# Optimization experiments

Measured on AMD Instinct MI355X. Metric: run time of the kernel, lower is better.

Reference implementation:

```python
import jax, jax.numpy as jnp
import numpy as np

HID, SD, EXP, DTR = 1024, 16, 2048, 64
B_, T_ = 4, 2048


def setup_inputs() -> dict:
    key = jax.random.key(0)
    ks = jax.random.split(key, 9)
    def rn(k, shape, s=0.02):
        return jax.random.normal(k, shape, jnp.float32) * s
    return {
        "x": jax.random.normal(ks[0], (B_, T_, HID), jnp.float32),
        "ln_g": jnp.ones((HID,), jnp.float32),
        "ln_b": jnp.zeros((HID,), jnp.float32),
        "W_in": rn(ks[1], (HID, 2 * EXP)),
        "b_in": jnp.zeros((2 * EXP,), jnp.float32),
        "W_del": rn(ks[2], (EXP, DTR)),
        "b_del": jnp.zeros((DTR,), jnp.float32),
        "W_dt": rn(ks[3], (DTR, EXP)),
        "b_dt": jnp.zeros((EXP,), jnp.float32),
        "W_B": rn(ks[4], (EXP, SD)),
        "b_B": jnp.zeros((SD,), jnp.float32),
        "W_C": rn(ks[5], (EXP, SD)),
        "b_C": jnp.zeros((SD,), jnp.float32),
        "A_log": -jnp.exp(0.1 * jax.random.normal(ks[6], (EXP, SD), jnp.float32)),
        "Dp": jnp.zeros((EXP,), jnp.float32),
        "W_out": rn(ks[7], (EXP, HID)),
        "b_out": jnp.zeros((HID,), jnp.float32),
    }


def _layernorm(x, g, b, eps=1e-5):
    m = jnp.mean(x, axis=-1, keepdims=True)
    v = jnp.var(x, axis=-1, keepdims=True)
    return (x - m) * jax.lax.rsqrt(v + eps) * g + b


def _selective_scan(u, delta, A, Bm, Cm):
    # u, delta: (B,T,E); Bm, Cm: (B,T,Sd); A: (E,Sd)
    def step(h, inp):
        u_t, d_t, B_t, C_t = inp  # (B,E),(B,E),(B,Sd),(B,Sd)
        A_disc = jnp.exp(d_t[..., None] * A[None])          # (B,E,Sd)
        h = A_disc * h + d_t[..., None] * B_t[:, None, :] * u_t[..., None]
        y_t = jnp.einsum("bs,bds->bd", C_t, h)
        return h, y_t
    h0 = jnp.zeros((u.shape[0], u.shape[2], A.shape[1]), u.dtype)
    xs = (u.transpose(1, 0, 2), delta.transpose(1, 0, 2),
          Bm.transpose(1, 0, 2), Cm.transpose(1, 0, 2))
    _, ys = jax.lax.scan(step, h0, xs)  # ys: (T,B,E)
    return ys.transpose(1, 0, 2)


def reference(x, ln_g, ln_b, W_in, b_in, W_del, b_del, W_dt, b_dt,
              W_B, b_B, W_C, b_C, A_log, Dp, W_out, b_out):
    res = x
    xn = _layernorm(x, ln_g, ln_b)
    xp = xn @ W_in + b_in                 # (B,T,2E)
    u, gate = jnp.split(xp, 2, axis=-1)   # each (B,T,E)
    u = jax.nn.silu(u)
    delta = jax.nn.softplus((u @ W_del + b_del) @ W_dt + b_dt)  # (B,T,E)
    Bm = u @ W_B + b_B                    # (B,T,Sd)
    Cm = u @ W_C + b_C                    # (B,T,Sd)
    A = -jnp.exp(A_log)                   # (E,Sd)
    y = _selective_scan(u, delta, A, Bm, Cm)
    y = y + u * Dp
    y = y * jax.nn.silu(gate)
    return y @ W_out + b_out + res
```

## Files before the change

kernel.cpp:

```cpp
#include <hip/hip_runtime.h>

#define HIDN 1024
#define EXPN 2048
#define SDIM 16
#define DTRN 64
#define BBN  4
#define TTN  2048
#define MMN  (BBN*TTN)
#define NCHUNK 32
#define CLEN (TTN/NCHUNK)
#define KSPL 8
#define KCH  (EXPN/KSPL)

typedef unsigned short u16;
typedef __bf16 bf16x8 __attribute__((ext_vector_type(8)));
typedef float f32x4 __attribute__((ext_vector_type(4)));

static __device__ __forceinline__ float b2f(u16 u) {
    union { unsigned int i; float f; } cv; cv.i = ((unsigned int)u) << 16; return cv.f;
}
static __device__ __forceinline__ u16 f2b(float f) {
    union { float f; unsigned int i; } cv; cv.f = f;
    unsigned int x = cv.i;
    return (u16)((x + 0x7fffu + ((x >> 16) & 1u)) >> 16);
}
static __device__ __forceinline__ float fexp2(float x) {
    return __builtin_amdgcn_exp2f(x);
}

static __device__ __forceinline__
void tr_tile(const float* __restrict__ W, u16* __restrict__ Wt,
             int K, int N, int bk, int bn, float (*t)[65]) {
    const int r0 = threadIdx.x >> 4, c0 = (threadIdx.x & 15) << 2;
    #pragma unroll
    for (int i = 0; i < 4; ++i) {
        float4 v = *(const float4*)(W + (size_t)(bk + r0 + i * 16) * N + bn + c0);
        t[r0 + i * 16][c0 + 0] = v.x; t[r0 + i * 16][c0 + 1] = v.y;
        t[r0 + i * 16][c0 + 2] = v.z; t[r0 + i * 16][c0 + 3] = v.w;
    }
    __syncthreads();
    #pragma unroll
    for (int i = 0; i < 4; ++i) {
        const int n = r0 + i * 16;
        ushort4 o;
        o.x = f2b(t[c0 + 0][n]); o.y = f2b(t[c0 + 1][n]);
        o.z = f2b(t[c0 + 2][n]); o.w = f2b(t[c0 + 3][n]);
        *(ushort4*)(Wt + (size_t)(bn + n) * K + bk + c0) = o;
    }
}

__global__ __launch_bounds__(256)
void k_prep(const float* __restrict__ W_in, const float* __restrict__ W_out,
            const float* __restrict__ W_dt, const float* __restrict__ W_del,
            const float* __restrict__ W_B, const float* __restrict__ W_C,
            const float* __restrict__ A_log,
            u16* __restrict__ Wt_in, u16* __restrict__ Wt_out,
            u16* __restrict__ Wdt_t, u16* __restrict__ Wcat,
            float* __restrict__ A2) {
    __shared__ float t[64][65];
    int blk = blockIdx.x;
    if (blk < 1024) {
        tr_tile(W_in, Wt_in, HIDN, 2 * EXPN, (blk >> 6) << 6, (blk & 63) << 6, t);
        return;
    }
    blk -= 1024;
    if (blk < 512) {
        tr_tile(W_out, Wt_out, EXPN, HIDN, (blk >> 4) << 6, (blk & 15) << 6, t);
        return;
    }
    blk -= 512;
    if (blk < 32) {
        tr_tile(W_dt, Wdt_t, DTRN, EXPN, 0, blk << 6, t);
        return;
    }
    blk -= 32;
    if (blk < 768) {
        const int i = blk * 256 + threadIdx.x;
        const int n = i >> 11, k = i & 2047;
        float v;
        if (n < 64)      v = W_del[(size_t)k * DTRN + n];
        else if (n < 80) v = W_B[(size_t)k * SDIM + (n - 64)];
        else             v = W_C[(size_t)k * SDIM + (n - 80)];
        Wcat[i] = f2b(v);
        return;
    }
    blk -= 768;
    {
        const int i = blk * 256 + threadIdx.x;
        A2[i] = -__expf(A_log[i]) * 1.44269504088896340736f;
    }
}

__global__ __launch_bounds__(256) void k_ln(const float* __restrict__ x,
                                            const float* __restrict__ g,
                                            const float* __restrict__ bta,
                                            u16* __restrict__ xn) {
    const int row = blockIdx.x, tid = threadIdx.x;
    const float4 xv = ((const float4*)(x + (size_t)row * HIDN))[tid];
    float s  = xv.x + xv.y + xv.z + xv.w;
    float ss = fmaf(xv.x, xv.x, fmaf(xv.y, xv.y, fmaf(xv.z, xv.z, xv.w * xv.w)));
    #pragma unroll
    for (int o = 32; o > 0; o >>= 1) { s += __shfl_down(s, o); ss += __shfl_down(ss, o); }
    __shared__ float as[4], bs[4];
    const int wid = tid >> 6, lane = tid & 63;
    if (lane == 0) { as[wid] = s; bs[wid] = ss; }
    __syncthreads();
    const float S  = as[0] + as[1] + as[2] + as[3];
    const float SS = bs[0] + bs[1] + bs[2] + bs[3];
    const float mean = S * (1.f / HIDN);
    const float var  = SS * (1.f / HIDN) - mean * mean;
    const float r = rsqrtf(var + 1e-5f);
    const float4 gv = ((const float4*)g)[tid];
    const float4 bv = ((const float4*)bta)[tid];
    ushort4 o;
    o.x = f2b((xv.x - mean) * r * gv.x + bv.x);
    o.y = f2b((xv.y - mean) * r * gv.y + bv.y);
    o.z = f2b((xv.z - mean) * r * gv.z + bv.z);
    o.w = f2b((xv.w - mean) * r * gv.w + bv.w);
    ((ushort4*)(xn + (size_t)row * HIDN))[tid] = o;
}

#define MEPI_SPLIT_SILU 0
#define MEPI_OUT        1
#define MEPI_SP         2

static __device__ __forceinline__
void stage256(const u16* __restrict__ A, const u16* __restrict__ Bt,
              u16 (*seg)[8192], int brow, int bcol, int K, int k0,
              const int* srow, const int* scol, int tid) {
    #pragma unroll
    for (int j = 0; j < 2; ++j) {
        #pragma unroll
        for (int h = 0; h < 2; ++h) {
            const u16* sa = A + (size_t)(brow + h * 128 + srow[j]) * K + k0 + scol[j];
            __builtin_amdgcn_global_load_lds(
                (const __attribute__((address_space(1))) void*)sa,
                (__attribute__((address_space(3))) void*)&seg[h][(j * 512 + tid) * 8], 16, 0, 0);
            const u16* sb = Bt + (size_t)(bcol + h * 128 + srow[j]) * K + k0 + scol[j];
            __builtin_amdgcn_global_load_lds(
                (const __attribute__((address_space(1))) void*)sb,
                (__attribute__((address_space(3))) void*)&seg[2 + h][(j * 512 + tid) * 8], 16, 0, 0);
        }
    }
}

template<int EPI>
__global__ __launch_bounds__(512, 2)
void mgemm256(const u16* __restrict__ A, const u16* __restrict__ Bt,
              const float* __restrict__ bias, void* __restrict__ O0,
              void* __restrict__ O1, const float* __restrict__ res,
              int N, int K) {
    __shared__ u16 lds[2][4][8192];
    const int tid  = threadIdx.x;
    const int lane = tid & 63, wid = tid >> 6;
    const int wm = wid >> 2, wn = wid & 3;
    const int r  = lane & 15, kh = lane >> 4;
    const int brow = blockIdx.y * 256, bcol = blockIdx.x * 256;

    int srow[2], scol[2];
    #pragma unroll
    for (int j = 0; j < 2; ++j) {
        const int q = j * 512 + tid;
        const int sub = q >> 6, qi = q & 63;
        const int qis = qi ^ (((qi >> 5) & 1) << 1);
        srow[j] = (sub >> 1) * 16 + (qi >> 2);
        scol[j] = ((sub & 1) << 5) + (qis & 3) * 8;
    }
    const int swz_kh = kh ^ (((r >> 3) & 1) << 1);
    const int rbase  = r * 32 + swz_kh * 8;
    const int bq     = wn & 1;

    f32x4 acc[8][4];
    #pragma unroll
    for (int i = 0; i < 8; ++i)
        #pragma unroll
        for (int n = 0; n < 4; ++n) acc[i][n] = (f32x4){0.f, 0.f, 0.f, 0.f};

    const int NT = K >> 6;
    stage256(A, Bt, lds[0], brow, bcol, K, 0, srow, scol, tid);
    stage256(A, Bt, lds[1], brow, bcol, K, 64, srow, scol, tid);
    asm volatile("s_waitcnt vmcnt(8)" ::: "memory");
    __builtin_amdgcn_s_barrier();
    asm volatile("" ::: "memory");

    bf16x8 a[4][2], b[2][2][2];
    for (int kt = 0; kt < NT; ++kt) {
        const u16* segA = lds[kt & 1][wm];
        const u16* segB = lds[kt & 1][2 + (wn >> 1)];
        #pragma unroll
        for (int mf = 0; mf < 4; ++mf)
            #pragma unroll
            for (int kk = 0; kk < 2; ++kk)
                a[mf][kk] = *(const bf16x8*)&segA[(mf * 2 + kk) * 512 + rbase];
        #pragma unroll
        for (int nf = 0; nf < 2; ++nf)
            #pragma unroll
            for (int kk = 0; kk < 2; ++kk)
                b[0][nf][kk] = *(const bf16x8*)&segB[((bq * 4 + nf) * 2 + kk) * 512 + rbase];
        __builtin_amdgcn_s_barrier(); asm volatile("" ::: "memory");
        __builtin_amdgcn_s_setprio(1);
        #pragma unroll
        for (int mf = 0; mf < 4; ++mf)
            #pragma unroll
            for (int nf = 0; nf < 2; ++nf)
                #pragma unroll
                for (int kk = 0; kk < 2; ++kk)
                    acc[mf][nf] = __builtin_amdgcn_mfma_f32_16x16x32_bf16(a[mf][kk], b[0][nf][kk], acc[mf][nf], 0, 0, 0);
        __builtin_amdgcn_s_setprio(0);
        __builtin_amdgcn_s_barrier(); asm volatile("" ::: "memory");
        #pragma unroll
        for (int nf = 0; nf < 2; ++nf)
            #pragma unroll
            for (int kk = 0; kk < 2; ++kk)
                b[1][nf][kk] = *(const bf16x8*)&segB[((bq * 4 + 2 + nf) * 2 + kk) * 512 + rbase];
        __builtin_amdgcn_s_barrier(); asm volatile("" ::: "memory");
        __builtin_amdgcn_s_setprio(1);
        #pragma unroll
        for (int mf = 0; mf < 4; ++mf)
            #pragma unroll
            for (int nf = 0; nf < 2; ++nf)
                #pragma unroll
                for (int kk = 0; kk < 2; ++kk)
                    acc[mf][2 + nf] = __builtin_amdgcn_mfma_f32_16x16x32_bf16(a[mf][kk], b[1][nf][kk], acc[mf][2 + nf], 0, 0, 0);
        __builtin_amdgcn_s_setprio(0);
        __builtin_amdgcn_s_barrier(); asm volatile("" ::: "memory");
        #pragma unroll
        for (int mf = 0; mf < 4; ++mf)
            #pragma unroll
            for (int kk = 0; kk < 2; ++kk)
                a[mf][kk] = *(const bf16x8*)&segA[((4 + mf) * 2 + kk) * 512 + rbase];
        __builtin_amdgcn_s_barrier(); asm volatile("" ::: "memory");
        __builtin_amdgcn_s_setprio(1);
        #pragma unroll
        for (int mf = 0; mf < 4; ++mf)
            #pragma unroll
            for (int nf = 0; nf < 2; ++nf)
                #pragma unroll
                for (int kk = 0; kk < 2; ++kk)
                    acc[4 + mf][nf] = __builtin_amdgcn_mfma_f32_16x16x32_bf16(a[mf][kk], b[0][nf][kk], acc[4 + mf][nf], 0, 0, 0);
        __builtin_amdgcn_s_setprio(0);
        __builtin_amdgcn_s_barrier(); asm volatile("" ::: "memory");
        if (kt + 2 < NT)
            stage256(A, Bt, lds[kt & 1], brow, bcol, K, (kt + 2) * 64, srow, scol, tid);
        __builtin_amdgcn_s_setprio(1);
        #pragma unroll
        for (int mf = 0; mf < 4; ++mf)
            #pragma unroll
            for (int nf = 0; nf < 2; ++nf)
                #pragma unroll
                for (int kk = 0; kk < 2; ++kk)
                    acc[4 + mf][2 + nf] = __builtin_amdgcn_mfma_f32_16x16x32_bf16(a[mf][kk], b[1][nf][kk], acc[4 + mf][2 + nf], 0, 0, 0);
        __builtin_amdgcn_s_setprio(0);
        if (kt + 2 < NT) { asm volatile("s_waitcnt vmcnt(8)" ::: "memory"); }
        else             { asm volatile("s_waitcnt vmcnt(0)" ::: "memory"); }
        __builtin_amdgcn_s_barrier(); asm volatile("" ::: "memory");
    }

    const int orow = brow + wm * 128 + kh * 4;
    const int ocol = bcol + wn * 64 + r;
    if constexpr (EPI == MEPI_SPLIT_SILU) {
        u16* dst; int cb;
        if (bcol < EXPN) { dst = (u16*)O0; cb = ocol; }
        else             { dst = (u16*)O1; cb = ocol - EXPN; }
        #pragma unroll
        for (int Mf = 0; Mf < 8; ++Mf)
            #pragma unroll
            for (int Nf = 0; Nf < 4; ++Nf)
                #pragma unroll
                for (int j = 0; j < 4; ++j) {
                    const int row = orow + Mf * 16 + j;
                    const int col = ocol + Nf * 16;
                    float v = acc[Mf][Nf][j] + bias[col];
                    float sv = v * (1.f / (1.f + __expf(-v)));
                    dst[(size_t)row * EXPN + cb + Nf * 16] = f2b(sv);
                }
    } else {
        float* o = (float*)O0;
        #pragma unroll
        for (int Mf = 0; Mf < 8; ++Mf)
            #pragma unroll
            for (int Nf = 0; Nf < 4; ++Nf)
                #pragma unroll
                for (int j = 0; j < 4; ++j) {
                    const int row = orow + Mf * 16 + j;
                    const int col = ocol + Nf * 16;
                    o[(size_t)row * N + col] = acc[Mf][Nf][j] + bias[col] + res[(size_t)row * N + col];
                }
    }
}

template<int EPI>
__global__ __launch_bounds__(256)
void mgemm(const u16* __restrict__ A, const u16* __restrict__ Bt,
           const float* __restrict__ bias, void* __restrict__ O0,
           void* __restrict__ O1, const float* __restrict__ res,
           int N, int K) {
    __shared__ u16 As[128 * 32];
    __shared__ u16 Bs[128 * 32];
    const int tid  = threadIdx.x;
    const int wave = tid >> 6, lane = tid & 63;
    const int brow = blockIdx.y * 128, bcol = blockIdx.x * 128;
    const int wm = wave >> 1, wn = wave & 1;
    const int r  = lane & 15, kh = lane >> 4;

    f32x4 acc[4][4];
    #pragma unroll
    for (int m = 0; m < 4; m++)
        #pragma unroll
        for (int n = 0; n < 4; n++) acc[m][n] = (f32x4){0.f, 0.f, 0.f, 0.f};

    const u16* ga0 = A  + (size_t)(brow +      (tid >> 2)) * K + (tid & 3) * 8;
    const u16* ga1 = A  + (size_t)(brow + 64 + (tid >> 2)) * K + (tid & 3) * 8;
    const u16* gb0 = Bt + (size_t)(bcol +      (tid >> 2)) * K + (tid & 3) * 8;
    const u16* gb1 = Bt + (size_t)(bcol + 64 + (tid >> 2)) * K + (tid & 3) * 8;
    u16* lA0 = As + (wave * 64) * 8;
    u16* lA1 = As + (256 + wave * 64) * 8;
    u16* lB0 = Bs + (wave * 64) * 8;
    u16* lB1 = Bs + (256 + wave * 64) * 8;

    for (int k0 = 0; k0 < K; k0 += 32) {
        __syncthreads();
        __builtin_amdgcn_global_load_lds((const __attribute__((address_space(1))) void*)(ga0 + k0),
                                         (__attribute__((address_space(3))) void*)lA0, 16, 0, 0);
        __builtin_amdgcn_global_load_lds((const __attribute__((address_space(1))) void*)(ga1 + k0),
                                         (__attribute__((address_space(3))) void*)lA1, 16, 0, 0);
        __builtin_amdgcn_global_load_lds((const __attribute__((address_space(1))) void*)(gb0 + k0),
                                         (__attribute__((address_space(3))) void*)lB0, 16, 0, 0);
        __builtin_amdgcn_global_load_lds((const __attribute__((address_space(1))) void*)(gb1 + k0),
                                         (__attribute__((address_space(3))) void*)lB1, 16, 0, 0);
        __syncthreads();
        bf16x8 af[4], bfr[4];
        #pragma unroll
        for (int mf = 0; mf < 4; ++mf)
            af[mf] = *(const bf16x8*)(As + ((wm * 64 + mf * 16 + r) * 32 + kh * 8));
        #pragma unroll
        for (int nf = 0; nf < 4; ++nf)
            bfr[nf] = *(const bf16x8*)(Bs + ((wn * 64 + nf * 16 + r) * 32 + kh * 8));
        #pragma unroll
        for (int mf = 0; mf < 4; ++mf)
            #pragma unroll
            for (int nf = 0; nf < 4; ++nf)
                acc[mf][nf] = __builtin_amdgcn_mfma_f32_16x16x32_bf16(af[mf], bfr[nf], acc[mf][nf], 0, 0, 0);
    }

    const int orow = brow + wm * 64 + kh * 4;
    const int ocol = bcol + wn * 64 + r;
    if constexpr (EPI == MEPI_SPLIT_SILU) {
        u16* dst; int cb;
        if (bcol < EXPN) { dst = (u16*)O0; cb = ocol; }
        else             { dst = (u16*)O1; cb = ocol - EXPN; }
        #pragma unroll
        for (int mf = 0; mf < 4; ++mf)
            #pragma unroll
            for (int nf = 0; nf < 4; ++nf)
                #pragma unroll
                for (int j = 0; j < 4; ++j) {
                    const int row = orow + mf * 16 + j;
                    const int col = ocol + nf * 16;
                    float v = acc[mf][nf][j] + bias[col];
                    float sv = v * (1.f / (1.f + __expf(-v)));
                    dst[(size_t)row * EXPN + cb + nf * 16] = f2b(sv);
                }
    } else if constexpr (EPI == MEPI_SP) {
        u16* o = (u16*)O0;
        #pragma unroll
        for (int mf = 0; mf < 4; ++mf)
            #pragma unroll
            for (int nf = 0; nf < 4; ++nf)
                #pragma unroll
                for (int j = 0; j < 4; ++j) {
                    const int row = orow + mf * 16 + j;
                    const int col = ocol + nf * 16;
                    float v = acc[mf][nf][j] + bias[col];
                    float sp = (v > 20.f) ? v
                             : 0.69314718056f * __builtin_amdgcn_logf(
                                   1.f + fexp2(1.44269504089f * v));
                    o[(size_t)row * N + col] = f2b(sp);
                }
    } else {
        float* o = (float*)O0;
        #pragma unroll
        for (int mf = 0; mf < 4; ++mf)
            #pragma unroll
            for (int nf = 0; nf < 4; ++nf)
                #pragma unroll
                for (int j = 0; j < 4; ++j) {
                    const int row = orow + mf * 16 + j;
                    const int col = ocol + nf * 16;
                    o[(size_t)row * N + col] = acc[mf][nf][j] + bias[col] + res[(size_t)row * N + col];
                }
    }
}

__global__ __launch_bounds__(256)
void k_proj(const u16* __restrict__ A, const u16* __restrict__ Wcat,
            float* __restrict__ Ppart) {
    __shared__ u16 As[128 * 32];
    __shared__ u16 Bs[96 * 32];
    const int tid  = threadIdx.x;
    const int wave = tid >> 6, lane = tid & 63;
    const int brow = blockIdx.y * 128;
    const int ks   = blockIdx.x;
    const int r = lane & 15, kh = lane >> 4;

    f32x4 acc[2][6];
    #pragma unroll
    for (int m = 0; m < 2; m++)
        #pragma unroll
        for (int n = 0; n < 6; n++) acc[m][n] = (f32x4){0.f, 0.f, 0.f, 0.f};

    const u16* ga0 = A + (size_t)(brow +      (tid >> 2)) * EXPN + ks * KCH + (tid & 3) * 8;
    const u16* ga1 = A + (size_t)(brow + 64 + (tid >> 2)) * EXPN + ks * KCH + (tid & 3) * 8;
    const u16* gb0 = Wcat + (size_t)(tid >> 2) * EXPN + ks * KCH + (tid & 3) * 8;
    const u16* gb1 = Wcat + (size_t)(64 + (tid >> 2)) * EXPN + ks * KCH + (tid & 3) * 8;
    u16* lA0 = As + (wave * 64) * 8;
    u16* lA1 = As + (256 + wave * 64) * 8;
    u16* lB0 = Bs + (wave * 64) * 8;
    u16* lB1 = Bs + (256 + wave * 64) * 8;

    for (int k0 = 0; k0 < KCH; k0 += 32) {
        __syncthreads();
        __builtin_amdgcn_global_load_lds((const __attribute__((address_space(1))) void*)(ga0 + k0),
                                         (__attribute__((address_space(3))) void*)lA0, 16, 0, 0);
        __builtin_amdgcn_global_load_lds((const __attribute__((address_space(1))) void*)(ga1 + k0),
                                         (__attribute__((address_space(3))) void*)lA1, 16, 0, 0);
        __builtin_amdgcn_global_load_lds((const __attribute__((address_space(1))) void*)(gb0 + k0),
                                         (__attribute__((address_space(3))) void*)lB0, 16, 0, 0);
        if (tid < 128)
            __builtin_amdgcn_global_load_lds((const __attribute__((address_space(1))) void*)(gb1 + k0),
                                             (__attribute__((address_space(3))) void*)lB1, 16, 0, 0);
        __syncthreads();
        bf16x8 af[2], bfr[6];
        #pragma unroll
        for (int mf = 0; mf < 2; ++mf)
            af[mf] = *(const bf16x8*)(As + ((wave * 32 + mf * 16 + r) * 32 + kh * 8));
        #pragma unroll
        for (int nf = 0; nf < 6; ++nf)
            bfr[nf] = *(const bf16x8*)(Bs + ((nf * 16 + r) * 32 + kh * 8));
        #pragma unroll
        for (int mf = 0; mf < 2; ++mf)
            #pragma unroll
            for (int nf = 0; nf < 6; ++nf)
                acc[mf][nf] = __builtin_amdgcn_mfma_f32_16x16x32_bf16(af[mf], bfr[nf], acc[mf][nf], 0, 0, 0);
    }
    const int orow = brow + wave * 32 + kh * 4;
    #pragma unroll
    for (int mf = 0; mf < 2; ++mf)
        #pragma unroll
        for (int nf = 0; nf < 6; ++nf)
            #pragma unroll
            for (int j = 0; j < 4; ++j)
                Ppart[((size_t)ks * MMN + orow + mf * 16 + j) * 96 + nf * 16 + r] = acc[mf][nf][j];
}

__global__ __launch_bounds__(192)
void k_red(const float* __restrict__ Ppart, const float* __restrict__ b_del,
           const float* __restrict__ b_B, const float* __restrict__ b_C,
           u16* __restrict__ t1b, float* __restrict__ Bm, float* __restrict__ Cm) {
    const int tid = threadIdx.x;
    const int ri  = tid / 96, col = tid - ri * 96;
    const int row = blockIdx.x * 2 + ri;
    float s = 0.f;
    #pragma unroll
    for (int ks = 0; ks < KSPL; ++ks)
        s += Ppart[((size_t)ks * MMN + row) * 96 + col];
    if (col < 64)      t1b[(size_t)row * DTRN + col] = f2b(s + b_del[col]);
    else if (col < 80) Bm[(size_t)row * SDIM + col - 64] = s + b_B[col - 64];
    else               Cm[(size_t)row * SDIM + col - 80] = s + b_C[col - 80];
}

__global__ __launch_bounds__(256)
void k_scan1(const u16* __restrict__ ub, const u16* __restrict__ db,
             const float* __restrict__ Bm, const float* __restrict__ A2,
             float* __restrict__ hend, float* __restrict__ Pp) {
    const int e = blockIdx.x * 256 + threadIdx.x;
    const int c = blockIdx.y, b = blockIdx.z;
    float a2[SDIM], h[SDIM];
    {
        const float4* ap = (const float4*)(A2 + (size_t)e * SDIM);
        float4 v0 = ap[0], v1 = ap[1], v2 = ap[2], v3 = ap[3];
        a2[0]=v0.x; a2[1]=v0.y; a2[2]=v0.z; a2[3]=v0.w;
        a2[4]=v1.x; a2[5]=v1.y; a2[6]=v1.z; a2[7]=v1.w;
        a2[8]=v2.x; a2[9]=v2.y; a2[10]=v2.z; a2[11]=v2.w;
        a2[12]=v3.x; a2[13]=v3.y; a2[14]=v3.z; a2[15]=v3.w;
    }
    #pragma unroll
    for (int s = 0; s < SDIM; s++) h[s] = 0.f;
    float sumd = 0.f;
    const int t0 = c * CLEN;
    size_t rb = ((size_t)b * TTN + t0) * EXPN + e;
    size_t bb_ = ((size_t)b * TTN + t0) * SDIM;
    for (int tt = 0; tt < CLEN; ++tt) {
        const float d  = b2f(db[rb]);
        const float uv = b2f(ub[rb]);
        const float4* bp = (const float4*)(Bm + bb_);
        float4 b0 = bp[0], b1 = bp[1], b2v = bp[2], b3 = bp[3];
        float bv[SDIM] = { b0.x,b0.y,b0.z,b0.w, b1.x,b1.y,b1.z,b1.w,
                           b2v.x,b2v.y,b2v.z,b2v.w, b3.x,b3.y,b3.z,b3.w };
        const float du = d * uv;
        sumd += d;
        #pragma unroll
        for (int s = 0; s < SDIM; ++s) {
            float ad = fexp2(d * a2[s]);
            h[s] = fmaf(ad, h[s], du * bv[s]);
        }
        rb += EXPN; bb_ += SDIM;
    }
    size_t ob = ((size_t)(b * NCHUNK + c) * SDIM) * EXPN + e;
    #pragma unroll
    for (int s = 0; s < SDIM; ++s) {
        hend[ob + (size_t)s * EXPN] = h[s];
        Pp  [ob + (size_t)s * EXPN] = fexp2(a2[s] * sumd);
    }
}

__global__ __launch_bounds__(256)
void k_fix(const float* __restrict__ hend, const float* __restrict__ Pp,
           float* __restrict__ hinit) {
    const int i = blockIdx.x * 256 + threadIdx.x;
    const int b = blockIdx.y;
    float hi = 0.f;
    size_t base = ((size_t)b * NCHUNK) * SDIM * EXPN + i;
    for (int cc = 0; cc < NCHUNK; ++cc) {
        size_t idx = base + (size_t)cc * SDIM * EXPN;
        hinit[idx] = hi;
        hi = fmaf(Pp[idx], hi, hend[idx]);
    }
}

__global__ __launch_bounds__(256)
void k_scan2(const u16* __restrict__ ub, const u16* __restrict__ db,
             const u16* __restrict__ sgb, const float* __restrict__ Bm,
             const float* __restrict__ Cm, const float* __restrict__ A2,
             const float* __restrict__ hinit, const float* __restrict__ Dp,
             u16* __restrict__ yb) {
    const int e = blockIdx.x * 256 + threadIdx.x;
    const int c = blockIdx.y, b = blockIdx.z;
    float a2[SDIM], h[SDIM];
    {
        const float4* ap = (const float4*)(A2 + (size_t)e * SDIM);
        float4 v0 = ap[0], v1 = ap[1], v2 = ap[2], v3 = ap[3];
        a2[0]=v0.x; a2[1]=v0.y; a2[2]=v0.z; a2[3]=v0.w;
        a2[4]=v1.x; a2[5]=v1.y; a2[6]=v1.z; a2[7]=v1.w;
        a2[8]=v2.x; a2[9]=v2.y; a2[10]=v2.z; a2[11]=v2.w;
        a2[12]=v3.x; a2[13]=v3.y; a2[14]=v3.z; a2[15]=v3.w;
    }
    {
        size_t hb = ((size_t)(b * NCHUNK + c) * SDIM) * EXPN + e;
        #pragma unroll
        for (int s = 0; s < SDIM; s++) h[s] = hinit[hb + (size_t)s * EXPN];
    }
    const float dpe = Dp[e];
    const int t0 = c * CLEN;
    size_t rb = ((size_t)b * TTN + t0) * EXPN + e;
    size_t bb_ = ((size_t)b * TTN + t0) * SDIM;
    for (int tt = 0; tt < CLEN; ++tt) {
        const float d   = b2f(db[rb]);
        const float uv  = b2f(ub[rb]);
        const float sgv = b2f(sgb[rb]);
        const float4* bp = (const float4*)(Bm + bb_);
        const float4* cp = (const float4*)(Cm + bb_);
        float4 b0 = bp[0], b1 = bp[1], b2v = bp[2], b3 = bp[3];
        float4 c0 = cp[0], c1 = cp[1], c2v = cp[2], c3 = cp[3];
        float bv[SDIM] = { b0.x,b0.y,b0.z,b0.w, b1.x,b1.y,b1.z,b1.w,
                           b2v.x,b2v.y,b2v.z,b2v.w, b3.x,b3.y,b3.z,b3.w };
        float cv[SDIM] = { c0.x,c0.y,c0.z,c0.w, c1.x,c1.y,c1.z,c1.w,
                           c2v.x,c2v.y,c2v.z,c2v.w, c3.x,c3.y,c3.z,c3.w };
        const float du = d * uv;
        float yt = 0.f;
        #pragma unroll
        for (int s = 0; s < SDIM; ++s) {
            float ad = fexp2(d * a2[s]);
            h[s] = fmaf(ad, h[s], du * bv[s]);
            yt = fmaf(cv[s], h[s], yt);
        }
        yb[rb] = f2b(fmaf(uv, dpe, yt) * sgv);
        rb += EXPN; bb_ += SDIM;
    }
}

extern "C" void kernel_launch(void* const* d_in, const int* in_sizes, int n_in,
                              void* d_out, int out_size, void* d_ws, size_t ws_size,
                              hipStream_t stream) {
    const float* x     = (const float*)d_in[0];
    const float* ln_g  = (const float*)d_in[1];
    const float* ln_b  = (const float*)d_in[2];
    const float* W_in  = (const float*)d_in[3];
    const float* b_in  = (const float*)d_in[4];
    const float* W_del = (const float*)d_in[5];
    const float* b_del = (const float*)d_in[6];
    const float* W_dt  = (const float*)d_in[7];
    const float* b_dt  = (const float*)d_in[8];
    const float* W_B   = (const float*)d_in[9];
    const float* b_B   = (const float*)d_in[10];
    const float* W_C   = (const float*)d_in[11];
    const float* b_C   = (const float*)d_in[12];
    const float* A_log = (const float*)d_in[13];
    const float* Dp    = (const float*)d_in[14];
    const float* W_out = (const float*)d_in[15];
    const float* b_out = (const float*)d_in[16];
    float* out = (float*)d_out;

    char* p = (char*)d_ws;
    auto alloc = [&](size_t bytes) {
        char* r = p; p += (bytes + 255) & ~(size_t)255; return (void*)r;
    };
    u16* xn   = (u16*)alloc((size_t)MMN * HIDN * 2);
    u16* u    = (u16*)alloc((size_t)MMN * EXPN * 2);
    u16* sg   = (u16*)alloc((size_t)MMN * EXPN * 2);
    u16* dl   = (u16*)alloc((size_t)MMN * EXPN * 2);
    u16* y    = (u16*)alloc((size_t)MMN * EXPN * 2);
    u16* t1b  = (u16*)alloc((size_t)MMN * DTRN * 2);
    float* Bm = (float*)alloc((size_t)MMN * SDIM * 4);
    float* Cm = (float*)alloc((size_t)MMN * SDIM * 4);
    float* A2 = (float*)alloc((size_t)EXPN * SDIM * 4);
    u16* Wt_in  = (u16*)alloc((size_t)(2 * EXPN) * HIDN * 2);
    u16* Wt_out = (u16*)alloc((size_t)HIDN * EXPN * 2);
    u16* Wcat   = (u16*)alloc((size_t)96 * EXPN * 2);
    u16* Wdt_t  = (u16*)alloc((size_t)EXPN * DTRN * 2);
    const size_t hsz = (size_t)BBN * NCHUNK * EXPN * SDIM * 4;
    float* hend  = (float*)alloc(hsz);
    float* Pp    = (float*)alloc(hsz);
    float* hinit = (float*)alloc(hsz);
    float* Ppart = hend;

    k_prep<<<dim3(1024 + 512 + 32 + 768 + 128), 256, 0, stream>>>(
        W_in, W_out, W_dt, W_del, W_B, W_C, A_log, Wt_in, Wt_out, Wdt_t, Wcat, A2);
    k_ln<<<dim3(MMN), 256, 0, stream>>>(x, ln_g, ln_b, xn);

    mgemm256<MEPI_SPLIT_SILU><<<dim3(2 * EXPN / 256, MMN / 256), 512, 0, stream>>>(
        xn, Wt_in, b_in, u, sg, nullptr, 2 * EXPN, HIDN);
    k_proj<<<dim3(KSPL, MMN / 128), 256, 0, stream>>>(u, Wcat, Ppart);
    k_red<<<dim3(MMN / 2), 192, 0, stream>>>(Ppart, b_del, b_B, b_C, t1b, Bm, Cm);
    mgemm<MEPI_SP><<<dim3(EXPN / 128, MMN / 128), 256, 0, stream>>>(
        t1b, Wdt_t, b_dt, dl, nullptr, nullptr, EXPN, DTRN);
    k_scan1<<<dim3(EXPN / 256, NCHUNK, BBN), 256, 0, stream>>>(u, dl, Bm, A2, hend, Pp);
    k_fix<<<dim3(SDIM * EXPN / 256, BBN), 256, 0, stream>>>(hend, Pp, hinit);
    k_scan2<<<dim3(EXPN / 256, NCHUNK, BBN), 256, 0, stream>>>(u, dl, sg, Bm, Cm, A2, hinit, Dp, y);
    mgemm<MEPI_OUT><<<dim3(HIDN / 128, MMN / 128), 256, 0, stream>>>(
        y, Wt_out, b_out, out, nullptr, x, HIDN, EXPN);
}
```

Before: 307.1 us.

## Run 256x256 input GEMM with 1024 threads and simpler per-k-step schedule

The input-projection GEMM now launches 16 waves per block instead of 8. Each wave owns a 64x64 output tile rather than 128x64, which halves the accumulator registers and lets each thread stage a single 16-byte chunk per operand. The fine-grained interleaved barrier and LDS-load schedule is replaced by a simple loop over the two k-halves, with one barrier pair per tile. The SiLU epilogue now uses an exp2-based helper. This trades per-wave register pressure and schedule complexity for more waves to hide latency, at the risk of losing the previous LDS/MFMA overlap tuning.

```diff
diff --git a/kernel.cpp b/kernel.cpp
--- a/kernel.cpp
+++ b/kernel.cpp
@@ -26,6 +26,9 @@
 }
 static __device__ __forceinline__ float fexp2(float x) {
     return __builtin_amdgcn_exp2f(x);
+}
+static __device__ __forceinline__ float fsilu(float v) {
+    return v / (1.f + fexp2(-1.44269504088896f * v));
 }
 
 static __device__ __forceinline__
@@ -127,25 +130,22 @@
 static __device__ __forceinline__
 void stage256(const u16* __restrict__ A, const u16* __restrict__ Bt,
               u16 (*seg)[8192], int brow, int bcol, int K, int k0,
-              const int* srow, const int* scol, int tid) {
-    #pragma unroll
-    for (int j = 0; j < 2; ++j) {
-        #pragma unroll
-        for (int h = 0; h < 2; ++h) {
-            const u16* sa = A + (size_t)(brow + h * 128 + srow[j]) * K + k0 + scol[j];
-            __builtin_amdgcn_global_load_lds(
-                (const __attribute__((address_space(1))) void*)sa,
-                (__attribute__((address_space(3))) void*)&seg[h][(j * 512 + tid) * 8], 16, 0, 0);
-            const u16* sb = Bt + (size_t)(bcol + h * 128 + srow[j]) * K + k0 + scol[j];
-            __builtin_amdgcn_global_load_lds(
-                (const __attribute__((address_space(1))) void*)sb,
-                (__attribute__((address_space(3))) void*)&seg[2 + h][(j * 512 + tid) * 8], 16, 0, 0);
-        }
+              int srow, int scol, int tid) {
+    #pragma unroll
+    for (int h = 0; h < 2; ++h) {
+        const u16* sa = A + (size_t)(brow + h * 128 + srow) * K + k0 + scol;
+        __builtin_amdgcn_global_load_lds(
+            (const __attribute__((address_space(1))) void*)sa,
+            (__attribute__((address_space(3))) void*)&seg[h][tid * 8], 16, 0, 0);
+        const u16* sb = Bt + (size_t)(bcol + h * 128 + srow) * K + k0 + scol;
+        __builtin_amdgcn_global_load_lds(
+            (const __attribute__((address_space(1))) void*)sb,
+            (__attribute__((address_space(3))) void*)&seg[2 + h][tid * 8], 16, 0, 0);
     }
 }
 
 template<int EPI>
-__global__ __launch_bounds__(512, 2)
+__global__ __launch_bounds__(1024)
 void mgemm256(const u16* __restrict__ A, const u16* __restrict__ Bt,
               const float* __restrict__ bias, void* __restrict__ O0,
               void* __restrict__ O1, const float* __restrict__ res,
@@ -157,113 +157,69 @@
     const int r  = lane & 15, kh = lane >> 4;
     const int brow = blockIdx.y * 256, bcol = blockIdx.x * 256;
 
-    int srow[2], scol[2];
-    #pragma unroll
-    for (int j = 0; j < 2; ++j) {
-        const int q = j * 512 + tid;
+    int srow, scol;
+    {
+        const int q = tid;
         const int sub = q >> 6, qi = q & 63;
         const int qis = qi ^ (((qi >> 5) & 1) << 1);
-        srow[j] = (sub >> 1) * 16 + (qi >> 2);
-        scol[j] = ((sub & 1) << 5) + (qis & 3) * 8;
+        srow = (sub >> 1) * 16 + (qi >> 2);
+        scol = ((sub & 1) << 5) + (qis & 3) * 8;
     }
     const int swz_kh = kh ^ (((r >> 3) & 1) << 1);
     const int rbase  = r * 32 + swz_kh * 8;
-    const int bq     = wn & 1;
-
-    f32x4 acc[8][4];
-    #pragma unroll
-    for (int i = 0; i < 8; ++i)
+    const int am = wm & 1, bq = wn & 1;
+
+    f32x4 acc[4][4];
+    #pragma unroll
+    for (int i = 0; i < 4; ++i)
         #pragma unroll
         for (int n = 0; n < 4; ++n) acc[i][n] = (f32x4){0.f, 0.f, 0.f, 0.f};
 
     const int NT = K >> 6;
     stage256(A, Bt, lds[0], brow, bcol, K, 0, srow, scol, tid);
     stage256(A, Bt, lds[1], brow, bcol, K, 64, srow, scol, tid);
-    asm volatile("s_waitcnt vmcnt(8)" ::: "memory");
+    asm volatile("s_waitcnt vmcnt(4)" ::: "memory");
     __builtin_amdgcn_s_barrier();
     asm volatile("" ::: "memory");
 
-    bf16x8 a[4][2], b[2][2][2];
     for (int kt = 0; kt < NT; ++kt) {
-        const u16* segA = lds[kt & 1][wm];
+        const u16* segA = lds[kt & 1][wm >> 1];
         const u16* segB = lds[kt & 1][2 + (wn >> 1)];
         #pragma unroll
-        for (int mf = 0; mf < 4; ++mf)
-            #pragma unroll
-            for (int kk = 0; kk < 2; ++kk)
-                a[mf][kk] = *(const bf16x8*)&segA[(mf * 2 + kk) * 512 + rbase];
-        #pragma unroll
-        for (int nf = 0; nf < 2; ++nf)
-            #pragma unroll
-            for (int kk = 0; kk < 2; ++kk)
-                b[0][nf][kk] = *(const bf16x8*)&segB[((bq * 4 + nf) * 2 + kk) * 512 + rbase];
+        for (int kk = 0; kk < 2; ++kk) {
+            bf16x8 a[4], b[4];
+            #pragma unroll
+            for (int mf = 0; mf < 4; ++mf)
+                a[mf] = *(const bf16x8*)&segA[((am * 4 + mf) * 2 + kk) * 512 + rbase];
+            #pragma unroll
+            for (int nf = 0; nf < 4; ++nf)
+                b[nf] = *(const bf16x8*)&segB[((bq * 4 + nf) * 2 + kk) * 512 + rbase];
+            __builtin_amdgcn_s_setprio(1);
+            #pragma unroll
+            for (int mf = 0; mf < 4; ++mf)
+                #pragma unroll
+                for (int nf = 0; nf < 4; ++nf)
+                    acc[mf][nf] = __builtin_amdgcn_mfma_f32_16x16x32_bf16(a[mf], b[nf], acc[mf][nf], 0, 0, 0);
+            __builtin_amdgcn_s_setprio(0);
+        }
         __builtin_amdgcn_s_barrier(); asm volatile("" ::: "memory");
-        __builtin_amdgcn_s_setprio(1);
-        #pragma unroll
-        for (int mf = 0; mf < 4; ++mf)
-            #pragma unroll
-            for (int nf = 0; nf < 2; ++nf)
-                #pragma unroll
-                for (int kk = 0; kk < 2; ++kk)
-                    acc[mf][nf] = __builtin_amdgcn_mfma_f32_16x16x32_bf16(a[mf][kk], b[0][nf][kk], acc[mf][nf], 0, 0, 0);
-        __builtin_amdgcn_s_setprio(0);
+        if (kt + 2 < NT) {
+            stage256(A, Bt, lds[kt & 1], brow, bcol, K, (kt + 2) * 64, srow, scol, tid);
+            asm volatile("s_waitcnt vmcnt(4)" ::: "memory");
+        } else {
+            asm volatile("s_waitcnt vmcnt(0)" ::: "memory");
+        }
         __builtin_amdgcn_s_barrier(); asm volatile("" ::: "memory");
-        #pragma unroll
-        for (int nf = 0; nf < 2; ++nf)
-            #pragma unroll
-            for (int kk = 0; kk < 2; ++kk)
-                b[1][nf][kk] = *(const bf16x8*)&segB[((bq * 4 + 2 + nf) * 2 + kk) * 512 + rbase];
-        __builtin_amdgcn_s_barrier(); asm volatile("" ::: "memory");
-        __builtin_amdgcn_s_setprio(1);
-        #pragma unroll
-        for (int mf = 0; mf < 4; ++mf)
-            #pragma unroll
-            for (int nf = 0; nf < 2; ++nf)
-                #pragma unroll
-                for (int kk = 0; kk < 2; ++kk)
-                    acc[mf][2 + nf] = __builtin_amdgcn_mfma_f32_16x16x32_bf16(a[mf][kk], b[1][nf][kk], acc[mf][2 + nf], 0, 0, 0);
-        __builtin_amdgcn_s_setprio(0);
-        __builtin_amdgcn_s_barrier(); asm volatile("" ::: "memory");
-        #pragma unroll
-        for (int mf = 0; mf < 4; ++mf)
-            #pragma unroll
-            for (int kk = 0; kk < 2; ++kk)
-                a[mf][kk] = *(const bf16x8*)&segA[((4 + mf) * 2 + kk) * 512 + rbase];
-        __builtin_amdgcn_s_barrier(); asm volatile("" ::: "memory");
-        __builtin_amdgcn_s_setprio(1);
-        #pragma unroll
-        for (int mf = 0; mf < 4; ++mf)
-            #pragma unroll
-            for (int nf = 0; nf < 2; ++nf)
-                #pragma unroll
-                for (int kk = 0; kk < 2; ++kk)
-                    acc[4 + mf][nf] = __builtin_amdgcn_mfma_f32_16x16x32_bf16(a[mf][kk], b[0][nf][kk], acc[4 + mf][nf], 0, 0, 0);
-        __builtin_amdgcn_s_setprio(0);
-        __builtin_amdgcn_s_barrier(); asm volatile("" ::: "memory");
-        if (kt + 2 < NT)
-            stage256(A, Bt, lds[kt & 1], brow, bcol, K, (kt + 2) * 64, srow, scol, tid);
-        __builtin_amdgcn_s_setprio(1);
-        #pragma unroll
-        for (int mf = 0; mf < 4; ++mf)
-            #pragma unroll
-            for (int nf = 0; nf < 2; ++nf)
-                #pragma unroll
-                for (int kk = 0; kk < 2; ++kk)
-                    acc[4 + mf][2 + nf] = __builtin_amdgcn_mfma_f32_16x16x32_bf16(a[mf][kk], b[1][nf][kk], acc[4 + mf][2 + nf], 0, 0, 0);
-        __builtin_amdgcn_s_setprio(0);
-        if (kt + 2 < NT) { asm volatile("s_waitcnt vmcnt(8)" ::: "memory"); }
-        else             { asm volatile("s_waitcnt vmcnt(0)" ::: "memory"); }
-        __builtin_amdgcn_s_barrier(); asm volatile("" ::: "memory");
-    }
-
-    const int orow = brow + wm * 128 + kh * 4;
+    }
+
+    const int orow = brow + wm * 64 + kh * 4;
     const int ocol = bcol + wn * 64 + r;
     if constexpr (EPI == MEPI_SPLIT_SILU) {
         u16* dst; int cb;
         if (bcol < EXPN) { dst = (u16*)O0; cb = ocol; }
         else             { dst = (u16*)O1; cb = ocol - EXPN; }
         #pragma unroll
-        for (int Mf = 0; Mf < 8; ++Mf)
+        for (int Mf = 0; Mf < 4; ++Mf)
             #pragma unroll
             for (int Nf = 0; Nf < 4; ++Nf)
                 #pragma unroll
@@ -271,13 +227,12 @@
                     const int row = orow + Mf * 16 + j;
                     const int col = ocol + Nf * 16;
                     float v = acc[Mf][Nf][j] + bias[col];
-                    float sv = v * (1.f / (1.f + __expf(-v)));
-                    dst[(size_t)row * EXPN + cb + Nf * 16] = f2b(sv);
+                    dst[(size_t)row * EXPN + cb + Nf * 16] = f2b(fsilu(v));
                 }
     } else {
         float* o = (float*)O0;
         #pragma unroll
-        for (int Mf = 0; Mf < 8; ++Mf)
+        for (int Mf = 0; Mf < 4; ++Mf)
             #pragma unroll
             for (int Nf = 0; Nf < 4; ++Nf)
                 #pragma unroll
@@ -345,23 +300,7 @@
 
     const int orow = brow + wm * 64 + kh * 4;
     const int ocol = bcol + wn * 64 + r;
-    if constexpr (EPI == MEPI_SPLIT_SILU) {
-        u16* dst; int cb;
-        if (bcol < EXPN) { dst = (u16*)O0; cb = ocol; }
-        else             { dst = (u16*)O1; cb = ocol - EXPN; }
-        #pragma unroll
-        for (int mf = 0; mf < 4; ++mf)
-            #pragma unroll
-            for (int nf = 0; nf < 4; ++nf)
-                #pragma unroll
-                for (int j = 0; j < 4; ++j) {
-                    const int row = orow + mf * 16 + j;
-                    const int col = ocol + nf * 16;
-                    float v = acc[mf][nf][j] + bias[col];
-                    float sv = v * (1.f / (1.f + __expf(-v)));
-                    dst[(size_t)row * EXPN + cb + nf * 16] = f2b(sv);
-                }
-    } else if constexpr (EPI == MEPI_SP) {
+    if constexpr (EPI == MEPI_SP) {
         u16* o = (u16*)O0;
         #pragma unroll
         for (int mf = 0; mf < 4; ++mf)
@@ -628,7 +567,7 @@
         W_in, W_out, W_dt, W_del, W_B, W_C, A_log, Wt_in, Wt_out, Wdt_t, Wcat, A2);
     k_ln<<<dim3(MMN), 256, 0, stream>>>(x, ln_g, ln_b, xn);
 
-    mgemm256<MEPI_SPLIT_SILU><<<dim3(2 * EXPN / 256, MMN / 256), 512, 0, stream>>>(
+    mgemm256<MEPI_SPLIT_SILU><<<dim3(2 * EXPN / 256, MMN / 256), 1024, 0, stream>>>(
         xn, Wt_in, b_in, u, sg, nullptr, 2 * EXPN, HIDN);
     k_proj<<<dim3(KSPL, MMN / 128), 256, 0, stream>>>(u, Wcat, Ppart);
     k_red<<<dim3(MMN / 2), 192, 0, stream>>>(Ppart, b_del, b_B, b_C, t1b, Bm, Cm);
```

Measured after the change: 302.6 us. Within noise of the previous version (-1.5%).
